# Kernel tuning notes

Hardware: AMD Instinct MI355X
Metric: run time of the kernel (lower is better)

## Reference

```python
import jax, jax.numpy as jnp
import numpy as np

# --- hashgrid config (from __init__: num_levels=16, level_dim=4, base_res=2, log2_hashmap_size=19, desired_res=2048) ---
NUM_LEVELS = 16
LEVEL_DIM = 4
BASE_RES = 2
DESIRED_RES = 2048
TABLE_SIZE = 2 ** 19
_b = np.exp((np.log(DESIRED_RES) - np.log(BASE_RES)) / (NUM_LEVELS - 1))
SCALES = BASE_RES * _b ** np.arange(NUM_LEVELS) - 1.0          # instant-ngp per-level scale
RES = (np.ceil(SCALES) + 1).astype(np.int64)                   # per-level grid resolution
PRIME = np.uint32(2654435761)                                  # 2D spatial hash prime


def softplus10(x):
    return jax.nn.softplus(10.0 * x) / 10.0


def hash_encode(u, tables):
    """u: [P,2] in [0,1]; tables: [L, TABLE_SIZE, LEVEL_DIM]. Returns [P, L*LEVEL_DIM]."""
    outs = []
    for l in range(NUM_LEVELS):
        s = float(SCALES[l])
        res = int(RES[l])
        pos = u * s + 0.5
        pf = jnp.floor(pos)
        fr = pos - pf                      # bilinear fractions, [P,2]
        pi = pf.astype(jnp.int32)
        acc = None
        for dx in (0, 1):
            for dy in (0, 1):
                cx = pi[:, 0] + dx
                cy = pi[:, 1] + dy
                if res * res <= TABLE_SIZE:
                    idx = cy * res + cx                                   # dense level
                else:
                    idx = (cx.astype(jnp.uint32) ^ (cy.astype(jnp.uint32) * PRIME)) % jnp.uint32(TABLE_SIZE)
                    idx = idx.astype(jnp.int32)                           # hashed level
                wx = fr[:, 0] if dx else 1.0 - fr[:, 0]
                wy = fr[:, 1] if dy else 1.0 - fr[:, 1]
                term = tables[l][idx] * (wx * wy)[:, None]                # gather + bilerp
                acc = term if acc is None else acc + term
        outs.append(acc)
    return jnp.concatenate(outs, axis=-1)


def setup_inputs() -> dict:
    key = jax.random.key(0)
    ks = jax.random.split(key, 4)
    B, N, T = 4, 2048, 192
    x = jax.random.normal(ks[0], (B, N, T, 2), jnp.float32)
    embeddings = jax.random.normal(ks[1], (NUM_LEVELS, TABLE_SIZE, LEVEL_DIM), jnp.float32) * 1e-2
    W0 = jax.random.normal(ks[2], (64, 64), jnp.float32) / 8.0
    b0 = jnp.zeros((64,), jnp.float32)
    W1 = jax.random.normal(ks[3], (64, 1), jnp.float32) / 8.0
    b1 = jnp.zeros((1,), jnp.float32)
    return {"x": x, "embeddings": embeddings, "W0": W0, "b0": b0, "W1": W1, "b1": b1}


def reference(x, embeddings, W0, b0, W1, b1):
    B, N, T = x.shape[:3]
    xf = x.reshape(-1, T, 2)                       # [B*N, T, 2]
    rays_o = xf[:, 0]
    rd = xf[:, -1] - xf[:, 0]
    rd = rd / jnp.linalg.norm(rd, axis=-1, keepdims=True)
    z = jnp.linspace(0.0, 2.0, T)                  # [T]
    sample_dist = 1.0 / T
    xys = rays_o[:, None, :] + rd[:, None, :] * z[None, :, None]   # [B*N, T, 2]
    xys = jnp.clip(xys, -1.0, 1.0)                 # aabb clamp [-1,-1,1,1]
    u = (xys.reshape(-1, 2) + 1.0) * 0.5           # map [-bound,bound] -> [0,1], bound=1
    feats = hash_encode(u, embeddings)             # [P, 64]
    h = softplus10(feats @ W0 + b0)
    sigma = softplus10(h @ W1 + b1).reshape(-1, T) # [B*N, T]
    deltas = jnp.concatenate([jnp.full((1,), sample_dist, sigma.dtype), z[1:] - z[:-1]])  # [T]
    density = (deltas[None, :] * sigma).reshape(B, N, T)
    return density
```

## Files before the change

### kernel.cpp

```cpp
#include <hip/hip_runtime.h>
#include <cmath>
#include <algorithm>

#define NUM_LEVELS 16
#define TABLE_SIZE 524288
#define TMASK (TABLE_SIZE - 1)
#define HASH_PRIME 2654435761u
#define T_SAMPLES 192
#define BLOCK 256
#define PTS 64
#define CHUNK 4096

typedef _Float16 f16;
typedef f16 f16x4 __attribute__((ext_vector_type(4)));
typedef f16 f16x8 __attribute__((ext_vector_type(8)));
typedef float f32x4 __attribute__((ext_vector_type(4)));

struct LvlParams {
    float s[NUM_LEVELS];
    int   res[NUM_LEVELS];
    int   hashed[NUM_LEVELS];
    int   off[NUM_LEVELS];
    int   used[NUM_LEVELS];
};

__device__ __forceinline__ float softplus10(float x) {
    float t = 10.0f * x;
    float e = __expf(-fabsf(t));
    return (fmaxf(t, 0.0f) + __logf(1.0f + e)) * 0.1f;
}

__device__ __forceinline__ f16x4 lerp4h(f16x4 c00, f16x4 c01, f16x4 c10, f16x4 c11,
                                        float fx, float fy) {
    float gx = 1.0f - fx, gy = 1.0f - fy;
    f16 w00 = (f16)(gx * gy), w01 = (f16)(gx * fy);
    f16 w10 = (f16)(fx * gy), w11 = (f16)(fx * fy);
    f16x4 v00 = {w00, w00, w00, w00}, v01 = {w01, w01, w01, w01};
    f16x4 v10 = {w10, w10, w10, w10}, v11 = {w11, w11, w11, w11};
    return c00 * v00 + c01 * v01 + c10 * v10 + c11 * v11;
}

__device__ __forceinline__ f16x4 lerp4f(f32x4 c00, f32x4 c01, f32x4 c10, f32x4 c11,
                                        float fx, float fy) {
    float w00 = (1.0f - fx) * (1.0f - fy), w01 = (1.0f - fx) * fy;
    float w10 = fx * (1.0f - fy),          w11 = fx * fy;
    f32x4 a = c00 * w00 + c01 * w01 + c10 * w10 + c11 * w11;
    return __builtin_convertvector(a, f16x4);
}

__global__ void prep(const float* __restrict__ W0, f16* __restrict__ w0f) {
    const int t = threadIdx.x;
    #pragma unroll
    for (int i = 0; i < 16; ++i) {
        int f = t * 16 + i;
        int j = f & 7, lx = (f >> 3) & 15, q = (f >> 7) & 3, nt = (f >> 9) & 3, kc = f >> 11;
        int k = kc * 32 + q * 8 + j;
        int n = nt * 16 + lx;
        w0f[f] = (f16)W0[k * 64 + n];
    }
}

__global__ void prep_tables(const float* __restrict__ emb, f16* __restrict__ embq,
                            const LvlParams lp) {
    const int l    = blockIdx.y;
    const int used = lp.used[l];
    const int base = blockIdx.x * CHUNK;
    if (base >= used) return;
    const int t = threadIdx.x;
    const float* src = emb + ((size_t)l * TABLE_SIZE + base) * 4;
    f16* dst = embq + (size_t)(lp.off[l] + base) * 4;
    #pragma unroll
    for (int i = 0; i < 16; ++i) {
        int e = t + 256 * i;
        if (base + e < used) {
            f32x4 v = *(const f32x4*)(src + (size_t)e * 4);
            *(f16x4*)(dst + (size_t)e * 4) = __builtin_convertvector(v, f16x4);
        }
    }
}

template<bool QT>
__launch_bounds__(BLOCK, 8)
__global__ void nerf_fused(const float* __restrict__ x,
                           const float* __restrict__ emb,
                           const f16* __restrict__ embq,
                           const f16* __restrict__ w0f,
                           const float* __restrict__ b0,
                           const float* __restrict__ W1,
                           const float* __restrict__ b1,
                           float* __restrict__ out,
                           const LvlParams lp) {
    __shared__ __align__(16) f16 feT[NUM_LEVELS * PTS * 4];

    const int tid  = threadIdx.x;
    const int lane = tid & 63;
    const int w    = __builtin_amdgcn_readfirstlane(tid >> 6);

    const int ray = blockIdx.x / 3;
    const int t   = (blockIdx.x - ray * 3) * PTS + lane;

    const float2 o  = *(const float2*)(x + (size_t)ray * (T_SAMPLES * 2));
    const float2 ep = *(const float2*)(x + (size_t)ray * (T_SAMPLES * 2) + (T_SAMPLES - 1) * 2);
    float rdx = ep.x - o.x, rdy = ep.y - o.y;
    float inv = 1.0f / sqrtf(rdx * rdx + rdy * rdy);
    rdx *= inv; rdy *= inv;
    const float z = (float)((double)t * (2.0 / 191.0));
    float px = fminf(fmaxf(o.x + rdx * z, -1.0f), 1.0f);
    float py = fminf(fmaxf(o.y + rdy * z, -1.0f), 1.0f);
    const float ux = (px + 1.0f) * 0.5f;
    const float uy = (py + 1.0f) * 0.5f;

    const int l3h = lp.hashed[w + 12];

    if (QT) {
        f16x4 ca[4][4];
        float fxs[4], fys[4];
        #pragma unroll
        for (int li = 0; li < 4; ++li) {
            const int l = w + li * 4;
            const float s = lp.s[l];
            float posx = ux * s + 0.5f, posy = uy * s + 0.5f;
            float pfx = floorf(posx), pfy = floorf(posy);
            fxs[li] = posx - pfx; fys[li] = posy - pfy;
            int cx = (int)pfx, cy = (int)pfy;
            int i00, i01, i10, i11;
            if (li == 3 && l3h) {
                unsigned hy0 = (unsigned)cy * HASH_PRIME;
                unsigned hy1 = hy0 + HASH_PRIME;
                i00 = (int)(((unsigned)cx ^ hy0) & TMASK);
                i01 = (int)(((unsigned)cx ^ hy1) & TMASK);
                i10 = (int)(((unsigned)(cx + 1) ^ hy0) & TMASK);
                i11 = (int)(((unsigned)(cx + 1) ^ hy1) & TMASK);
            } else {
                const int res = lp.res[l];
                i00 = cy * res + cx; i10 = i00 + 1;
                i01 = i00 + res;     i11 = i01 + 1;
            }
            const f16x4* tb = (const f16x4*)embq + lp.off[l];
            ca[li][0] = tb[i00]; ca[li][1] = tb[i01];
            ca[li][2] = tb[i10]; ca[li][3] = tb[i11];
        }
        #pragma unroll
        for (int li = 0; li < 4; ++li) {
            const int l = w + li * 4;
            *(f16x4*)&feT[(l * PTS + lane) * 4] =
                lerp4h(ca[li][0], ca[li][1], ca[li][2], ca[li][3], fxs[li], fys[li]);
        }
    } else {
        #pragma unroll
        for (int li = 0; li < 4; ++li) {
            const int l = w + li * 4;
            const float s = lp.s[l];
            float posx = ux * s + 0.5f, posy = uy * s + 0.5f;
            float pfx = floorf(posx), pfy = floorf(posy);
            float fx = posx - pfx, fy = posy - pfy;
            int cx = (int)pfx, cy = (int)pfy;
            int i00, i01, i10, i11;
            if (li == 3 && l3h) {
                unsigned hy0 = (unsigned)cy * HASH_PRIME;
                unsigned hy1 = hy0 + HASH_PRIME;
                i00 = (int)(((unsigned)cx ^ hy0) & TMASK);
                i01 = (int)(((unsigned)cx ^ hy1) & TMASK);
                i10 = (int)(((unsigned)(cx + 1) ^ hy0) & TMASK);
                i11 = (int)(((unsigned)(cx + 1) ^ hy1) & TMASK);
            } else {
                const int res = lp.res[l];
                i00 = cy * res + cx; i10 = i00 + 1;
                i01 = i00 + res;     i11 = i01 + 1;
            }
            const f32x4* tb = (const f32x4*)(emb + (size_t)l * (TABLE_SIZE * 4));
            f32x4 a = tb[i00], b = tb[i01], c = tb[i10], d = tb[i11];
            *(f16x4*)&feT[(l * PTS + lane) * 4] = lerp4f(a, b, c, d, fx, fy);
        }
    }

    __syncthreads();

    const int lx = lane & 15, q = lane >> 4;
    const int p  = w * 16 + lx;

    f32x4 acc[4];
    #pragma unroll
    for (int nt = 0; nt < 4; ++nt) acc[nt] = (f32x4)(0.0f);

    #pragma unroll
    for (int kc = 0; kc < 2; ++kc) {
        const int la = kc * 8 + 2 * q;
        f16x4 lo = *(const f16x4*)&feT[(la * PTS + p) * 4];
        f16x4 hi = *(const f16x4*)&feT[((la + 1) * PTS + p) * 4];
        f16x8 afr = __builtin_shufflevector(lo, hi, 0, 1, 2, 3, 4, 5, 6, 7);
        #pragma unroll
        for (int nt = 0; nt < 4; ++nt) {
            f16x8 bfr = *(const f16x8*)(w0f + (size_t)(((kc * 4 + nt) * 4 + q) * 16 + lx) * 8);
            acc[nt] = __builtin_amdgcn_mfma_f32_16x16x32_f16(afr, bfr, acc[nt], 0, 0, 0);
        }
    }

    float b010[4], w1s[4];
    #pragma unroll
    for (int nt = 0; nt < 4; ++nt) {
        b010[nt] = b0[nt * 16 + lx] * 10.0f;
        w1s[nt]  = W1[nt * 16 + lx] * 0.1f;
    }
    const float b1v = b1[0];
    const float d0 = (float)(1.0 / 192.0);
    const float d1 = (float)(2.0 / 191.0);

    float part[4];
    #pragma unroll
    for (int r = 0; r < 4; ++r) {
        float pp = 0.0f;
        #pragma unroll
        for (int nt = 0; nt < 4; ++nt) {
            float t10 = fmaf(acc[nt][r], 10.0f, b010[nt]);
            float e   = __expf(-fabsf(t10));
            float sp  = fmaxf(t10, 0.0f) + __logf(1.0f + e);
            pp = fmaf(sp, w1s[nt], pp);
        }
        pp += __shfl_xor(pp, 1, 64);
        pp += __shfl_xor(pp, 2, 64);
        pp += __shfl_xor(pp, 4, 64);
        pp += __shfl_xor(pp, 8, 64);
        part[r] = pp;
    }
    if (lx == 0) {
        const int g0 = blockIdx.x * PTS + w * 16 + q * 4;
        const int tt = g0 % T_SAMPLES;
        f32x4 ov;
        ov.x = softplus10(part[0] + b1v) * (tt == 0 ? d0 : d1);
        ov.y = softplus10(part[1] + b1v) * d1;
        ov.z = softplus10(part[2] + b1v) * d1;
        ov.w = softplus10(part[3] + b1v) * d1;
        *(f32x4*)(out + g0) = ov;
    }
}

extern "C" void kernel_launch(void* const* d_in, const int* in_sizes, int n_in,
                              void* d_out, int out_size, void* d_ws, size_t ws_size,
                              hipStream_t stream) {
    const float* x   = (const float*)d_in[0];
    const float* emb = (const float*)d_in[1];
    const float* W0  = (const float*)d_in[2];
    const float* b0  = (const float*)d_in[3];
    const float* W1  = (const float*)d_in[4];
    const float* b1  = (const float*)d_in[5];
    float* out = (float*)d_out;

    char* ws = (char*)d_ws;
    f16* w0f  = (f16*)ws;
    f16* embq = (f16*)(ws + 16384);

    LvlParams lp;
    const double bb = std::exp((std::log(2048.0) - std::log(2.0)) / 15.0);
    int off = 0, maxUsed = 0;
    for (int l = 0; l < NUM_LEVELS; ++l) {
        double sc = 2.0 * std::pow(bb, (double)l) - 1.0;
        int rr = (int)std::ceil(sc) + 1;
        lp.s[l] = (float)sc;
        lp.res[l] = rr;
        lp.hashed[l] = ((long long)rr * (long long)rr > (long long)TABLE_SIZE) ? 1 : 0;
        int used;
        if (lp.hashed[l]) {
            used = TABLE_SIZE;
        } else {
            long long cmax = (long long)std::floor(sc + 0.5) + 1;
            long long u = cmax * (long long)rr + cmax + 1 + (rr + 2);
            used = (int)std::min((long long)TABLE_SIZE, u);
        }
        lp.off[l]  = off;
        lp.used[l] = used;
        off += (used + CHUNK - 1) & ~(CHUNK - 1);
        if (used > maxUsed) maxUsed = used;
    }
    const size_t need = 16384 + (size_t)off * 4 * sizeof(f16);
    const bool useQ = ws_size >= need;

    prep<<<1, 256, 0, stream>>>(W0, w0f);

    const int nblk = out_size / PTS;
    if (useQ) {
        dim3 pg((maxUsed + CHUNK - 1) / CHUNK, NUM_LEVELS);
        prep_tables<<<pg, 256, 0, stream>>>(emb, embq, lp);
        nerf_fused<true><<<nblk, BLOCK, 0, stream>>>(x, emb, embq, w0f,
                                                     b0, W1, b1, out, lp);
    } else {
        nerf_fused<false><<<nblk, BLOCK, 0, stream>>>(x, emb, embq, w0f,
                                                      b0, W1, b1, out, lp);
    }
}
```

Before: 343.3 us.

## Pre-pack dense grid cells as 2x2 corner quads for single-fetch bilerp

For dense (non-hashed) levels, the prep kernel now stores, for each cell, all four corner feature vectors contiguously as 32 bytes of fp16. The main kernel then fetches one corner quad with two 16-byte loads instead of four scattered 8-byte gathers. This is meant to cut the number of memory transactions and the cache-line misses in the gather phase. In exchange the dense tables take four times the workspace and prep_tables reads each source entry four times, and the fp16 path is skipped if the workspace is too small.

```diff
diff --git a/kernel.cpp b/kernel.cpp
--- a/kernel.cpp
+++ b/kernel.cpp
@@ -20,7 +20,7 @@
     float s[NUM_LEVELS];
     int   res[NUM_LEVELS];
     int   hashed[NUM_LEVELS];
-    int   off[NUM_LEVELS];
+    int   offB[NUM_LEVELS];
     int   used[NUM_LEVELS];
 };
 
@@ -60,21 +60,43 @@
     }
 }
 
-__global__ void prep_tables(const float* __restrict__ emb, f16* __restrict__ embq,
+__global__ void prep_tables(const float* __restrict__ emb, char* __restrict__ embq,
                             const LvlParams lp) {
     const int l    = blockIdx.y;
     const int used = lp.used[l];
     const int base = blockIdx.x * CHUNK;
     if (base >= used) return;
     const int t = threadIdx.x;
-    const float* src = emb + ((size_t)l * TABLE_SIZE + base) * 4;
-    f16* dst = embq + (size_t)(lp.off[l] + base) * 4;
-    #pragma unroll
-    for (int i = 0; i < 16; ++i) {
-        int e = t + 256 * i;
-        if (base + e < used) {
-            f32x4 v = *(const f32x4*)(src + (size_t)e * 4);
-            *(f16x4*)(dst + (size_t)e * 4) = __builtin_convertvector(v, f16x4);
+    const float* src = emb + (size_t)l * TABLE_SIZE * 4;
+    char* dst = embq + lp.offB[l];
+    if (lp.hashed[l]) {
+        #pragma unroll
+        for (int i = 0; i < 16; ++i) {
+            int e = base + t + 256 * i;
+            if (e < used) {
+                f32x4 v = *(const f32x4*)(src + (size_t)e * 4);
+                *(f16x4*)(dst + (size_t)e * 8) = __builtin_convertvector(v, f16x4);
+            }
+        }
+    } else {
+        const int res = lp.res[l];
+        #pragma unroll
+        for (int i = 0; i < 16; ++i) {
+            int e = base + t + 256 * i;
+            if (e < used) {
+                f32x4 v00 = *(const f32x4*)(src + (size_t)e * 4);
+                f32x4 v10 = *(const f32x4*)(src + (size_t)(e + 1) * 4);
+                f32x4 v01 = *(const f32x4*)(src + (size_t)(e + res) * 4);
+                f32x4 v11 = *(const f32x4*)(src + (size_t)(e + res + 1) * 4);
+                f16x4 a = __builtin_convertvector(v00, f16x4);
+                f16x4 b = __builtin_convertvector(v10, f16x4);
+                f16x4 c = __builtin_convertvector(v01, f16x4);
+                f16x4 d = __builtin_convertvector(v11, f16x4);
+                f16x8 q0 = __builtin_shufflevector(a, b, 0, 1, 2, 3, 4, 5, 6, 7);
+                f16x8 q1 = __builtin_shufflevector(c, d, 0, 1, 2, 3, 4, 5, 6, 7);
+                *(f16x8*)(dst + ((size_t)e << 5))      = q0;
+                *(f16x8*)(dst + ((size_t)e << 5) + 16) = q1;
+            }
         }
     }
 }
@@ -83,7 +105,7 @@
 __launch_bounds__(BLOCK, 8)
 __global__ void nerf_fused(const float* __restrict__ x,
                            const float* __restrict__ emb,
-                           const f16* __restrict__ embq,
+                           const char* __restrict__ embq,
                            const f16* __restrict__ w0f,
                            const float* __restrict__ b0,
                            const float* __restrict__ W1,
@@ -113,7 +135,7 @@
     const int l3h = lp.hashed[w + 12];
 
     if (QT) {
-        f16x4 ca[4][4];
+        f16x4 c00[4], c01[4], c10[4], c11[4];
         float fxs[4], fys[4];
         #pragma unroll
         for (int li = 0; li < 4; ++li) {
@@ -123,28 +145,33 @@
             float pfx = floorf(posx), pfy = floorf(posy);
             fxs[li] = posx - pfx; fys[li] = posy - pfy;
             int cx = (int)pfx, cy = (int)pfy;
-            int i00, i01, i10, i11;
+            const char* lb = embq + lp.offB[l];
             if (li == 3 && l3h) {
                 unsigned hy0 = (unsigned)cy * HASH_PRIME;
                 unsigned hy1 = hy0 + HASH_PRIME;
-                i00 = (int)(((unsigned)cx ^ hy0) & TMASK);
-                i01 = (int)(((unsigned)cx ^ hy1) & TMASK);
-                i10 = (int)(((unsigned)(cx + 1) ^ hy0) & TMASK);
-                i11 = (int)(((unsigned)(cx + 1) ^ hy1) & TMASK);
+                int iA  = (int)(((unsigned)cx ^ hy0) & TMASK);
+                int iB  = (int)(((unsigned)cx ^ hy1) & TMASK);
+                int iA1 = (int)(((unsigned)(cx + 1) ^ hy0) & TMASK);
+                int iB1 = (int)(((unsigned)(cx + 1) ^ hy1) & TMASK);
+                c00[li] = *(const f16x4*)(lb + ((size_t)iA  << 3));
+                c01[li] = *(const f16x4*)(lb + ((size_t)iB  << 3));
+                c10[li] = *(const f16x4*)(lb + ((size_t)iA1 << 3));
+                c11[li] = *(const f16x4*)(lb + ((size_t)iB1 << 3));
             } else {
-                const int res = lp.res[l];
-                i00 = cy * res + cx; i10 = i00 + 1;
-                i01 = i00 + res;     i11 = i01 + 1;
+                int i00 = cy * lp.res[l] + cx;
+                f16x8 q0 = *(const f16x8*)(lb + ((size_t)i00 << 5));
+                f16x8 q1 = *(const f16x8*)(lb + ((size_t)i00 << 5) + 16);
+                c00[li] = __builtin_shufflevector(q0, q0, 0, 1, 2, 3);
+                c10[li] = __builtin_shufflevector(q0, q0, 4, 5, 6, 7);
+                c01[li] = __builtin_shufflevector(q1, q1, 0, 1, 2, 3);
+                c11[li] = __builtin_shufflevector(q1, q1, 4, 5, 6, 7);
             }
-            const f16x4* tb = (const f16x4*)embq + lp.off[l];
-            ca[li][0] = tb[i00]; ca[li][1] = tb[i01];
-            ca[li][2] = tb[i10]; ca[li][3] = tb[i11];
         }
         #pragma unroll
         for (int li = 0; li < 4; ++li) {
             const int l = w + li * 4;
             *(f16x4*)&feT[(l * PTS + lane) * 4] =
-                lerp4h(ca[li][0], ca[li][1], ca[li][2], ca[li][3], fxs[li], fys[li]);
+                lerp4h(c00[li], c01[li], c10[li], c11[li], fxs[li], fys[li]);
         }
     } else {
         #pragma unroll
@@ -247,12 +274,12 @@
     float* out = (float*)d_out;
 
     char* ws = (char*)d_ws;
-    f16* w0f  = (f16*)ws;
-    f16* embq = (f16*)(ws + 16384);
+    f16*  w0f  = (f16*)ws;
+    char* embq = ws + 16384;
 
     LvlParams lp;
     const double bb = std::exp((std::log(2048.0) - std::log(2.0)) / 15.0);
-    int off = 0, maxUsed = 0;
+    int offB = 0, maxUsed = 0;
     for (int l = 0; l < NUM_LEVELS; ++l) {
         double sc = 2.0 * std::pow(bb, (double)l) - 1.0;
         int rr = (int)std::ceil(sc) + 1;
@@ -267,12 +294,13 @@
             long long u = cmax * (long long)rr + cmax + 1 + (rr + 2);
             used = (int)std::min((long long)TABLE_SIZE, u);
         }
-        lp.off[l]  = off;
+        lp.offB[l] = offB;
         lp.used[l] = used;
-        off += (used + CHUNK - 1) & ~(CHUNK - 1);
+        const long long bytes = lp.hashed[l] ? (long long)used * 8 : (long long)used * 32;
+        offB += (int)((bytes + 4095) & ~4095LL);
         if (used > maxUsed) maxUsed = used;
     }
-    const size_t need = 16384 + (size_t)off * 4 * sizeof(f16);
+    const size_t need = 16384 + (size_t)offB;
     const bool useQ = ws_size >= need;
 
     prep<<<1, 256, 0, stream>>>(W0, w0f);
```

New measurement: 351.6 us. 1.02x slower.
